# Kernel optimization log

Hardware: AMD Instinct MI355X
Metric: run time of the kernel (lower is better)

## Reference

```python
import jax, jax.numpy as jnp
import numpy as np

N_NODES = 50000
NEG_SLOPE = 0.2  # PyG GATConv default
EPS = 1e-16      # PyG softmax denominator epsilon


def _gat_conv(x, edge_index, W, att_src, att_dst, bias):
    """Single-head PyG-style GATConv with self-loops.
    x: [N, F_in], edge_index: [2, E] (row 0 = src/j, row 1 = dst/i).
    """
    n = x.shape[0]
    loop = jnp.arange(n, dtype=edge_index.dtype)
    src = jnp.concatenate([edge_index[0], loop])  # [E+N]
    dst = jnp.concatenate([edge_index[1], loop])  # [E+N]

    h = x @ W                                      # [N, F_out]
    a_src = h @ att_src                            # [N]
    a_dst = h @ att_dst                            # [N]

    e = jax.nn.leaky_relu(a_src[src] + a_dst[dst], NEG_SLOPE)  # [E+N]
    # segment softmax over incoming edges of each dst node
    m = jax.ops.segment_max(e, dst, num_segments=n)
    m = jnp.where(jnp.isfinite(m), m, 0.0)
    e = jnp.exp(e - m[dst])
    s = jax.ops.segment_sum(e, dst, num_segments=n)
    alpha = e / (s[dst] + EPS)                     # [E+N]

    out = jax.ops.segment_sum(alpha[:, None] * h[src], dst, num_segments=n)
    return out + bias


def setup_inputs() -> dict:
    key = jax.random.key(0)
    ks = jax.random.split(key, 10)
    d_in, d_hid, d_emb = 128, 64, 64
    n_edges = 800000
    x = jax.random.normal(ks[0], (N_NODES, d_in), dtype=jnp.float32)
    edge_index = jax.random.randint(ks[1], (2, n_edges), 0, N_NODES, dtype=jnp.int64)
    def glorot(k, shape):
        lim = float(np.sqrt(6.0 / sum(shape)))
        return jax.random.uniform(k, shape, jnp.float32, -lim, lim)
    return {
        "x": x,
        "edge_index": edge_index,
        "W1": glorot(ks[2], (d_in, d_hid)),
        "att_src1": glorot(ks[3], (d_hid,)),
        "att_dst1": glorot(ks[4], (d_hid,)),
        "b1": jnp.zeros((d_hid,), jnp.float32),
        "W2": glorot(ks[5], (d_hid, d_emb)),
        "att_src2": glorot(ks[6], (d_emb,)),
        "att_dst2": glorot(ks[7], (d_emb,)),
        "b2": jnp.zeros((d_emb,), jnp.float32),
    }


def reference(x, edge_index, W1, att_src1, att_dst1, b1, W2, att_src2, att_dst2, b2):
    x1 = jax.nn.relu(_gat_conv(x, edge_index, W1, att_src1, att_dst1, b1))
    # dropout is identity in eval mode
    x2 = _gat_conv(x1, edge_index, W2, att_src2, att_dst2, b2)
    return x2
```

## Files before the change

### kernel.cpp

```cpp
#include <hip/hip_runtime.h>
#include <hip/hip_bf16.h>

#define F_OUT 64
#define NEG_SLOPE 0.2f
#define SOFT_EPS 1e-16f
#define BW 256
#define CH 8192
#define TH 512

typedef short short8 __attribute__((ext_vector_type(8)));
typedef float floatx4 __attribute__((ext_vector_type(4)));
typedef unsigned short ushort4v __attribute__((ext_vector_type(4)));

__device__ __forceinline__ unsigned short f2bf_bits(float v) {
    __hip_bfloat16 hb = __float2bfloat16(v);
    return *(unsigned short*)&hb;
}
__device__ __forceinline__ float bf_bits2f(unsigned short u) {
    __hip_bfloat16 hb = *(__hip_bfloat16*)&u;
    return __bfloat162float(hb);
}
__device__ __forceinline__ float read_any(const void* src, int off, int bf) {
    return bf ? __bfloat162float(((const __hip_bfloat16*)src)[off])
              : ((const float*)src)[off];
}
__device__ __forceinline__ int get_idx(const void* ei, int i64, long long pos) {
    return i64 ? (int)((const long long*)ei)[pos] : ((const int*)ei)[pos];
}

__device__ __forceinline__ void detect_local(const unsigned* wbits, const unsigned* ebits,
                                             int* sm_bf, int* sm_i64) {
    if (threadIdx.x < 64) {
        unsigned w = wbits[threadIdx.x];
        unsigned e = (w >> 7) & 0xFFu;
        unsigned long long mb = __ballot(e >= 0x60u && e <= 0x7Eu);
        unsigned long long mz = __ballot(ebits[2 * threadIdx.x + 1] == 0u);
        if (threadIdx.x == 0) { *sm_bf = (__popcll(mb) > 32); *sm_i64 = (__popcll(mz) > 32); }
    }
    __syncthreads();
}

__global__ void count_prep(const void* __restrict__ ei, int* __restrict__ table,
                           const void* w1, const void* as1, const void* ad1, const void* b1,
                           const void* w2, const void* as2, const void* ad2, const void* b2,
                           unsigned short* __restrict__ wt1, unsigned short* __restrict__ wt2,
                           float* __restrict__ vecs, int* __restrict__ flags,
                           int E, int total, int NB, int nchunks, int n1, int n2, int K1) {
    __shared__ int cnt[1024];
    __shared__ int s_bf, s_i64;
    detect_local((const unsigned*)w1, (const unsigned*)ei, &s_bf, &s_i64);
    int bf = s_bf, i64 = s_i64;
    int g = blockIdx.x, tid = threadIdx.x;
    if (g == 0 && tid == 0) { flags[0] = bf; flags[1] = i64; }

    if (g < nchunks) {
        for (int k = tid; k < NB; k += TH) cnt[k] = 0;
        __syncthreads();
        int base = g * CH;
        int lim = base + CH < total ? base + CH : total;
        for (int t = base + tid; t < lim; t += TH) {
            int i = t < E ? get_idx(ei, i64, (long long)E + t) : t - E;
            atomicAdd(&cnt[i >> 8], 1);
        }
        __syncthreads();
        for (int k = tid; k < NB; k += TH) table[k * nchunks + g] = cnt[k];
    } else {
        int wtotal = n1 + n2 + 384;
        for (int t = tid; t < wtotal; t += TH) {
            if (t < n1) {
                int n = t / K1, k = t - n * K1;
                wt1[t] = f2bf_bits(read_any(w1, k * F_OUT + n, bf));
            } else if (t < n1 + n2) {
                int u = t - n1;
                int n = u >> 6, k = u & 63;
                wt2[u] = f2bf_bits(read_any(w2, k * F_OUT + n, bf));
            } else {
                int u = t - n1 - n2;
                const void* srcp[6] = {as1, ad1, b1, as2, ad2, b2};
                vecs[u] = read_any(srcp[u >> 6], u & 63, bf);
            }
        }
    }
}

template <int K, int WAVES>
__device__ __forceinline__ void gemm_body(int blk, int tid,
                          const void* __restrict__ xv, const unsigned short* __restrict__ Wt,
                          const float* __restrict__ att_s, const float* __restrict__ att_d,
                          unsigned short* __restrict__ h, float* __restrict__ a_s,
                          float* __restrict__ a_d, int N, int bf) {
    int lane = tid & 63;
    int m0 = (blk * WAVES + (tid >> 6)) * 16;
    if (m0 >= N) return;
    int c = lane & 15, quad = lane >> 4;
    int arow = m0 + c;
    if (arow >= N) arow = N - 1;

    floatx4 acc0 = {0.f, 0.f, 0.f, 0.f};
    floatx4 acc1 = acc0, acc2 = acc0, acc3 = acc0;

    for (int kc = 0; kc < K; kc += 32) {
        int ka = kc + quad * 8;
        short8 a;
        if (bf) {
            a = *(const short8*)((const unsigned short*)xv + (size_t)arow * K + ka);
        } else {
            const float* xp = (const float*)xv + (size_t)arow * K + ka;
#pragma unroll
            for (int j = 0; j < 8; ++j) a[j] = (short)f2bf_bits(xp[j]);
        }
        short8 b0 = *(const short8*)(Wt + (size_t)(c)      * K + ka);
        short8 b1 = *(const short8*)(Wt + (size_t)(16 + c) * K + ka);
        short8 b2 = *(const short8*)(Wt + (size_t)(32 + c) * K + ka);
        short8 b3 = *(const short8*)(Wt + (size_t)(48 + c) * K + ka);
        acc0 = __builtin_amdgcn_mfma_f32_16x16x32_bf16(a, b0, acc0, 0, 0, 0);
        acc1 = __builtin_amdgcn_mfma_f32_16x16x32_bf16(a, b1, acc1, 0, 0, 0);
        acc2 = __builtin_amdgcn_mfma_f32_16x16x32_bf16(a, b2, acc2, 0, 0, 0);
        acc3 = __builtin_amdgcn_mfma_f32_16x16x32_bf16(a, b3, acc3, 0, 0, 0);
    }

    float as0 = att_s[c],      as1 = att_s[16 + c], as2 = att_s[32 + c], as3 = att_s[48 + c];
    float ad0 = att_d[c],      ad1 = att_d[16 + c], ad2 = att_d[32 + c], ad3 = att_d[48 + c];
#pragma unroll
    for (int reg = 0; reg < 4; ++reg) {
        int row = m0 + quad * 4 + reg;
        float vs = acc0[reg] * as0 + acc1[reg] * as1 + acc2[reg] * as2 + acc3[reg] * as3;
        float vd = acc0[reg] * ad0 + acc1[reg] * ad1 + acc2[reg] * ad2 + acc3[reg] * ad3;
#pragma unroll
        for (int off = 1; off < 16; off <<= 1) {
            vs += __shfl_xor(vs, off);
            vd += __shfl_xor(vd, off);
        }
        if (row < N) {
            if (c == 0) { a_s[row] = vs; a_d[row] = vd; }
            unsigned short* hr = h + (size_t)row * F_OUT + c;
            hr[0]  = f2bf_bits(acc0[reg]);
            hr[16] = f2bf_bits(acc1[reg]);
            hr[32] = f2bf_bits(acc2[reg]);
            hr[48] = f2bf_bits(acc3[reg]);
        }
    }
}

__global__ void __launch_bounds__(TH)
scatter_gemm1(const void* __restrict__ ei, const int* __restrict__ table,
              unsigned* __restrict__ staged, int* __restrict__ segbeg,
              int* __restrict__ row_ptr, const void* __restrict__ xv,
              const unsigned short* __restrict__ Wt,
              const float* __restrict__ att_s, const float* __restrict__ att_d,
              unsigned short* __restrict__ h, float* __restrict__ a_s,
              float* __restrict__ a_d, const unsigned* __restrict__ wbits,
              int E, int total, int NB, int nchunks, int N) {
    __shared__ int s_bf, s_i64;
    detect_local(wbits, (const unsigned*)ei, &s_bf, &s_i64);
    int tid = threadIdx.x;
    if ((int)blockIdx.x >= nchunks) {
        gemm_body<128, 8>(blockIdx.x - nchunks, tid, xv, Wt, att_s, att_d,
                          h, a_s, a_d, N, s_bf);
        return;
    }
    __shared__ int s_scan[TH];
    __shared__ int s_cur[1024];
    int g = blockIdx.x;
    int i64 = s_i64;
    int b0 = 0;
    if (tid < NB) {
        const int* row = table + (size_t)tid * nchunks;
        int rsum = 0, rpart = 0;
        for (int c2 = 0; c2 < nchunks; ++c2) {
            int v = row[c2];
            rsum += v;
            rpart += (c2 < g) ? v : 0;
        }
        b0 = rsum;
        s_cur[tid] = rpart;
    }
    s_scan[tid] = (tid < NB) ? b0 : 0;
    __syncthreads();
    for (int off = 1; off < TH; off <<= 1) {
        int v = (tid >= off) ? s_scan[tid - off] : 0;
        __syncthreads();
        s_scan[tid] += v;
        __syncthreads();
    }
    if (tid < NB) {
        int excl = s_scan[tid] - b0;
        s_cur[tid] = excl + s_cur[tid];
        if (g == 0) segbeg[tid] = excl;
    }
    if (g == 0 && tid == 0) { segbeg[NB] = total; row_ptr[N] = total; }
    __syncthreads();
    int base = g * CH;
    int lim = base + CH < total ? base + CH : total;
    for (int t = base + tid; t < lim; t += TH) {
        int i = t < E ? get_idx(ei, i64, (long long)E + t) : t - E;
        int j = t < E ? get_idx(ei, i64, t) : t - E;
        int pos = atomicAdd(&s_cur[i >> 8], 1);
        staged[pos] = ((unsigned)(i & 255) << 24) | (unsigned)j;
    }
}

__global__ void bucket_csr(const unsigned* __restrict__ staged, const int* __restrict__ segbeg,
                           int* __restrict__ row_ptr, int* __restrict__ eidx, int N) {
    __shared__ int ldeg[BW];
    __shared__ int lcur[BW];
    __shared__ int wtot[4];
    int b = blockIdx.x;
    int t = threadIdx.x;
    int seg_beg = segbeg[b];
    int seg_end = segbeg[b + 1];
    ldeg[t] = 0;
    __syncthreads();
    for (int p = seg_beg + t; p < seg_end; p += 256)
        atomicAdd(&ldeg[staged[p] >> 24], 1);
    __syncthreads();
    int lane = t & 63, w = t >> 6;
    int d = ldeg[t];
    int v = d;
#pragma unroll
    for (int off = 1; off < 64; off <<= 1) {
        int u = __shfl_up(v, off);
        if (lane >= off) v += u;
    }
    if (lane == 63) wtot[w] = v;
    __syncthreads();
    int woff = 0;
    for (int k = 0; k < w; ++k) woff += wtot[k];
    int excl = v - d + woff;
    int node = b * BW + t;
    if (node < N) row_ptr[node] = seg_beg + excl;
    lcur[t] = excl;
    __syncthreads();
    for (int p = seg_beg + t; p < seg_end; p += 256) {
        unsigned pk = staged[p];
        int pos = atomicAdd(&lcur[pk >> 24], 1);
        eidx[seg_beg + pos] = (int)(pk & 0xFFFFFFu);
    }
}

__device__ __forceinline__ void gather_node(int i, int lane, int quad, int c,
                                            const int* __restrict__ row_ptr,
                                            const int* __restrict__ eidx,
                                            const float* __restrict__ a_s,
                                            const float* __restrict__ a_d,
                                            const unsigned short* __restrict__ h,
                                            float* se_out, floatx4* A_out) {
    int beg = row_ptr[i];
    int end = row_ptr[i + 1];
    float ad = a_d[i];
    float se = 0.f;
    floatx4 acc[4];
#pragma unroll
    for (int k = 0; k < 4; ++k) acc[k] = (floatx4){0.f, 0.f, 0.f, 0.f};

    for (int p = beg; p < end; p += 64) {
        int tile = end - p; if (tile > 64) tile = 64;
        int jm = eidx[p + (lane < tile ? lane : tile - 1)];
        float wm = 0.f;
        if (lane < tile) {
            float e = a_s[jm] + ad;
            wm = __expf(e > 0.f ? e : NEG_SLOPE * e);
        }
        se += wm;
        for (int e = 0; e < tile; e += 16) {
#pragma unroll
            for (int k = 0; k < 4; ++k) {
                if (e + 4 * k < tile) {
                    int idx = e + 4 * k + quad;
                    int srcl = idx < tile ? idx : tile - 1;
                    int jk = __shfl(jm, srcl);
                    float wk = __shfl(wm, srcl);
                    if (idx >= tile) wk = 0.f;
                    ushort4v hv = *(const ushort4v*)(h + (size_t)jk * F_OUT + (c << 2));
                    acc[k][0] += wk * bf_bits2f(hv[0]);
                    acc[k][1] += wk * bf_bits2f(hv[1]);
                    acc[k][2] += wk * bf_bits2f(hv[2]);
                    acc[k][3] += wk * bf_bits2f(hv[3]);
                }
            }
        }
    }
#pragma unroll
    for (int off = 1; off < 64; off <<= 1) se += __shfl_xor(se, off);
    floatx4 A = (acc[0] + acc[1]) + (acc[2] + acc[3]);
#pragma unroll
    for (int m = 0; m < 4; ++m) {
        A[m] += __shfl_xor(A[m], 16);
        A[m] += __shfl_xor(A[m], 32);
    }
    *se_out = se;
    *A_out = A;
}

#define XST 72
__global__ void __launch_bounds__(1024)
gather1_gemm2(const int* __restrict__ row_ptr, const int* __restrict__ eidx,
              const float* __restrict__ a_s, const float* __restrict__ a_d,
              const unsigned short* __restrict__ h, const float* __restrict__ bias,
              const unsigned short* __restrict__ Wt2,
              const float* __restrict__ att_s2, const float* __restrict__ att_d2,
              unsigned short* __restrict__ h2, float* __restrict__ a_s2,
              float* __restrict__ a_d2, int N) {
    __shared__ unsigned short x1t[16 * XST];
    int tid = threadIdx.x;
    int lane = tid & 63;
    int wv = tid >> 6;
    int quad = lane >> 4, c = lane & 15;
    int i = blockIdx.x * 16 + wv;

    if (i < N) {
        float se; floatx4 A;
        gather_node(i, lane, quad, c, row_ptr, eidx, a_s, a_d, h, &se, &A);
        if (quad == 0) {
            int col = c << 2;
            float inv = 1.f / (se + SOFT_EPS);
            float v0 = A[0] * inv + bias[col];
            float v1 = A[1] * inv + bias[col + 1];
            float v2 = A[2] * inv + bias[col + 2];
            float v3 = A[3] * inv + bias[col + 3];
            ushort4v ov;
            ov[0] = f2bf_bits(v0 > 0.f ? v0 : 0.f);
            ov[1] = f2bf_bits(v1 > 0.f ? v1 : 0.f);
            ov[2] = f2bf_bits(v2 > 0.f ? v2 : 0.f);
            ov[3] = f2bf_bits(v3 > 0.f ? v3 : 0.f);
            *(ushort4v*)(x1t + wv * XST + col) = ov;
        }
    } else if (quad == 0) {
        *(ushort4v*)(x1t + wv * XST + (c << 2)) = (ushort4v){0, 0, 0, 0};
    }
    __syncthreads();

    if (wv == 0) {
        int m0 = blockIdx.x * 16;
        floatx4 acc0 = {0.f, 0.f, 0.f, 0.f};
        floatx4 acc1 = acc0, acc2 = acc0, acc3 = acc0;
#pragma unroll
        for (int kc = 0; kc < 64; kc += 32) {
            int ka = kc + quad * 8;
            short8 a = *(const short8*)(x1t + c * XST + ka);
            short8 b0 = *(const short8*)(Wt2 + (size_t)(c)      * 64 + ka);
            short8 b1 = *(const short8*)(Wt2 + (size_t)(16 + c) * 64 + ka);
            short8 b2 = *(const short8*)(Wt2 + (size_t)(32 + c) * 64 + ka);
            short8 b3 = *(const short8*)(Wt2 + (size_t)(48 + c) * 64 + ka);
            acc0 = __builtin_amdgcn_mfma_f32_16x16x32_bf16(a, b0, acc0, 0, 0, 0);
            acc1 = __builtin_amdgcn_mfma_f32_16x16x32_bf16(a, b1, acc1, 0, 0, 0);
            acc2 = __builtin_amdgcn_mfma_f32_16x16x32_bf16(a, b2, acc2, 0, 0, 0);
            acc3 = __builtin_amdgcn_mfma_f32_16x16x32_bf16(a, b3, acc3, 0, 0, 0);
        }
        float as0 = att_s2[c],      as1 = att_s2[16 + c], as2 = att_s2[32 + c], as3 = att_s2[48 + c];
        float ad0 = att_d2[c],      ad1 = att_d2[16 + c], ad2 = att_d2[32 + c], ad3 = att_d2[48 + c];
#pragma unroll
        for (int reg = 0; reg < 4; ++reg) {
            int row = m0 + quad * 4 + reg;
            float vs = acc0[reg] * as0 + acc1[reg] * as1 + acc2[reg] * as2 + acc3[reg] * as3;
            float vd = acc0[reg] * ad0 + acc1[reg] * ad1 + acc2[reg] * ad2 + acc3[reg] * ad3;
#pragma unroll
            for (int off = 1; off < 16; off <<= 1) {
                vs += __shfl_xor(vs, off);
                vd += __shfl_xor(vd, off);
            }
            if (row < N) {
                if (c == 0) { a_s2[row] = vs; a_d2[row] = vd; }
                unsigned short* hr = h2 + (size_t)row * F_OUT + c;
                hr[0]  = f2bf_bits(acc0[reg]);
                hr[16] = f2bf_bits(acc1[reg]);
                hr[32] = f2bf_bits(acc2[reg]);
                hr[48] = f2bf_bits(acc3[reg]);
            }
        }
    }
}

__global__ void node_gather_out(const int* __restrict__ row_ptr, const int* __restrict__ eidx,
                                const float* __restrict__ a_s, const float* __restrict__ a_d,
                                const unsigned short* __restrict__ h, const float* __restrict__ bias,
                                void* __restrict__ out, int N, const int* __restrict__ flags) {
    int lane = threadIdx.x & 63;
    int i = blockIdx.x * 4 + (threadIdx.x >> 6);
    if (i >= N) return;
    int quad = lane >> 4, c = lane & 15;
    float se; floatx4 A;
    gather_node(i, lane, quad, c, row_ptr, eidx, a_s, a_d, h, &se, &A);
    if (quad == 0) {
        int col = c << 2;
        float inv = 1.f / (se + SOFT_EPS);
        float v0 = A[0] * inv + bias[col];
        float v1 = A[1] * inv + bias[col + 1];
        float v2 = A[2] * inv + bias[col + 2];
        float v3 = A[3] * inv + bias[col + 3];
        size_t o = (size_t)i * F_OUT + col;
        if (flags[0]) {
            ushort4v ov;
            ov[0] = f2bf_bits(v0); ov[1] = f2bf_bits(v1);
            ov[2] = f2bf_bits(v2); ov[3] = f2bf_bits(v3);
            *(ushort4v*)((unsigned short*)out + o) = ov;
        } else {
            floatx4 ov = {v0, v1, v2, v3};
            *(floatx4*)((float*)out + o) = ov;
        }
    }
}

extern "C" void kernel_launch(void* const* d_in, const int* in_sizes, int n_in,
                              void* d_out, int out_size, void* d_ws, size_t ws_size,
                              hipStream_t stream) {
    const void* x   = d_in[0];
    const void* ei  = d_in[1];
    const void* W1  = d_in[2];
    const void* as1 = d_in[3];
    const void* ad1 = d_in[4];
    const void* b1  = d_in[5];
    const void* W2  = d_in[6];
    const void* as2 = d_in[7];
    const void* ad2 = d_in[8];
    const void* b2  = d_in[9];

    int E  = in_sizes[1] / 2;
    int n1 = in_sizes[2];
    int n2 = in_sizes[6];
    int K1 = n1 / F_OUT;
    int N  = in_sizes[0] / K1;
    int total = E + N;
    int NB = (N + BW - 1) / BW;
    int nchunks = (total + CH - 1) / CH;
    int M = NB * nchunks;

    size_t nf = (size_t)N * F_OUT;
    char* wsb = (char*)d_ws;
    unsigned short* h   = (unsigned short*)wsb;
    unsigned short* h2  = h + nf;
    unsigned short* wt1 = h2 + nf;
    unsigned short* wt2 = wt1 + n1;
    float* a_s  = (float*)(wt2 + n2 + ((n1 + n2) & 1));
    float* a_d  = a_s + N;
    float* a_s2 = a_d + N;
    float* a_d2 = a_s2 + N;
    float* vecs = a_d2 + N;
    float* cAs1 = vecs,       *cAd1 = vecs + 64,  *cB1 = vecs + 128;
    float* cAs2 = vecs + 192, *cAd2 = vecs + 256, *cB2 = vecs + 320;
    int* flags    = (int*)(vecs + 384);
    int* row_ptr  = flags + 8;
    int* eidx     = row_ptr + N + 1;
    unsigned* staged = (unsigned*)(eidx + total);
    int* table    = (int*)(staged + total);
    int* segbeg   = table + M;

    int blkG1 = (N + 127) / 128;
    int blkFuse = (N + 15) / 16;
    int blkNode = (N + 3) / 4;

    count_prep<<<nchunks + 1, TH, 0, stream>>>(ei, table, W1, as1, ad1, b1,
                                               W2, as2, ad2, b2, wt1, wt2, vecs, flags,
                                               E, total, NB, nchunks, n1, n2, K1);
    scatter_gemm1<<<nchunks + blkG1, TH, 0, stream>>>(ei, table, staged, segbeg, row_ptr,
                                                      x, wt1, cAs1, cAd1, h, a_s, a_d,
                                                      (const unsigned*)W1,
                                                      E, total, NB, nchunks, N);
    bucket_csr<<<NB, 256, 0, stream>>>(staged, segbeg, row_ptr, eidx, N);
    gather1_gemm2<<<blkFuse, 1024, 0, stream>>>(row_ptr, eidx, a_s, a_d, h, cB1,
                                                wt2, cAs2, cAd2, h2, a_s2, a_d2, N);
    node_gather_out<<<blkNode, 256, 0, stream>>>(row_ptr, eidx, a_s2, a_d2, h2, cB2,
                                                 d_out, N, flags);
}
```

Baseline: 203.6 us.

## Split per-node edge gather into 8 edge groups with 16-byte feature loads

The per-node gather now gives each wave's 8 lane groups a contiguous slice of the node's incoming edges. Each lane loads 8 bf16 features at once and every lane computes its own attention weights, replacing the earlier tile-and-shuffle scheme that used 4-wide loads. Partial sums are combined with xor shuffles at the end. The CSR bucketing kernel also moves to 512 threads per block to speed up the scatter loops. The intent is fewer shuffles and wider memory transactions, at the cost of more redundant exp work per edge and possible imbalance on low-degree nodes.

```diff
diff --git a/kernel.cpp b/kernel.cpp
--- a/kernel.cpp
+++ b/kernel.cpp
@@ -7,10 +7,12 @@
 #define BW 256
 #define CH 8192
 #define TH 512
+#define TH3 512
 
 typedef short short8 __attribute__((ext_vector_type(8)));
 typedef float floatx4 __attribute__((ext_vector_type(4)));
 typedef unsigned short ushort4v __attribute__((ext_vector_type(4)));
+typedef unsigned short ushort8v __attribute__((ext_vector_type(8)));
 
 __device__ __forceinline__ unsigned short f2bf_bits(float v) {
     __hip_bfloat16 hb = __float2bfloat16(v);
@@ -200,8 +202,9 @@
     }
 }
 
-__global__ void bucket_csr(const unsigned* __restrict__ staged, const int* __restrict__ segbeg,
-                           int* __restrict__ row_ptr, int* __restrict__ eidx, int N) {
+__global__ void __launch_bounds__(TH3)
+bucket_csr(const unsigned* __restrict__ staged, const int* __restrict__ segbeg,
+           int* __restrict__ row_ptr, int* __restrict__ eidx, int N) {
     __shared__ int ldeg[BW];
     __shared__ int lcur[BW];
     __shared__ int wtot[4];
@@ -209,87 +212,89 @@
     int t = threadIdx.x;
     int seg_beg = segbeg[b];
     int seg_end = segbeg[b + 1];
-    ldeg[t] = 0;
-    __syncthreads();
-    for (int p = seg_beg + t; p < seg_end; p += 256)
+    if (t < BW) ldeg[t] = 0;
+    __syncthreads();
+    for (int p = seg_beg + t; p < seg_end; p += TH3)
         atomicAdd(&ldeg[staged[p] >> 24], 1);
     __syncthreads();
     int lane = t & 63, w = t >> 6;
-    int d = ldeg[t];
-    int v = d;
-#pragma unroll
-    for (int off = 1; off < 64; off <<= 1) {
-        int u = __shfl_up(v, off);
-        if (lane >= off) v += u;
-    }
-    if (lane == 63) wtot[w] = v;
-    __syncthreads();
-    int woff = 0;
-    for (int k = 0; k < w; ++k) woff += wtot[k];
-    int excl = v - d + woff;
-    int node = b * BW + t;
-    if (node < N) row_ptr[node] = seg_beg + excl;
-    lcur[t] = excl;
-    __syncthreads();
-    for (int p = seg_beg + t; p < seg_end; p += 256) {
+    int d = 0, v = 0;
+    if (t < BW) {
+        d = ldeg[t];
+        v = d;
+#pragma unroll
+        for (int off = 1; off < 64; off <<= 1) {
+            int u = __shfl_up(v, off);
+            if (lane >= off) v += u;
+        }
+        if (lane == 63) wtot[w] = v;
+    }
+    __syncthreads();
+    if (t < BW) {
+        int woff = 0;
+        for (int k = 0; k < w; ++k) woff += wtot[k];
+        int excl = v - d + woff;
+        int node = b * BW + t;
+        if (node < N) row_ptr[node] = seg_beg + excl;
+        lcur[t] = excl;
+    }
+    __syncthreads();
+    for (int p = seg_beg + t; p < seg_end; p += TH3) {
         unsigned pk = staged[p];
         int pos = atomicAdd(&lcur[pk >> 24], 1);
         eidx[seg_beg + pos] = (int)(pk & 0xFFFFFFu);
     }
 }
 
-__device__ __forceinline__ void gather_node(int i, int lane, int quad, int c,
-                                            const int* __restrict__ row_ptr,
-                                            const int* __restrict__ eidx,
-                                            const float* __restrict__ a_s,
-                                            const float* __restrict__ a_d,
-                                            const unsigned short* __restrict__ h,
-                                            float* se_out, floatx4* A_out) {
+__device__ __forceinline__ void gather_node8(int i, int grp, int c8,
+                                             const int* __restrict__ row_ptr,
+                                             const int* __restrict__ eidx,
+                                             const float* __restrict__ a_s,
+                                             const float* __restrict__ a_d,
+                                             const unsigned short* __restrict__ h,
+                                             float* se_out, float acc[8]) {
     int beg = row_ptr[i];
     int end = row_ptr[i + 1];
+    int len = end - beg;
     float ad = a_d[i];
+    int gb = beg + ((len * grp) >> 3);
+    int ge = beg + ((len * (grp + 1)) >> 3);
     float se = 0.f;
-    floatx4 acc[4];
-#pragma unroll
-    for (int k = 0; k < 4; ++k) acc[k] = (floatx4){0.f, 0.f, 0.f, 0.f};
-
-    for (int p = beg; p < end; p += 64) {
-        int tile = end - p; if (tile > 64) tile = 64;
-        int jm = eidx[p + (lane < tile ? lane : tile - 1)];
-        float wm = 0.f;
-        if (lane < tile) {
-            float e = a_s[jm] + ad;
-            wm = __expf(e > 0.f ? e : NEG_SLOPE * e);
-        }
-        se += wm;
-        for (int e = 0; e < tile; e += 16) {
-#pragma unroll
-            for (int k = 0; k < 4; ++k) {
-                if (e + 4 * k < tile) {
-                    int idx = e + 4 * k + quad;
-                    int srcl = idx < tile ? idx : tile - 1;
-                    int jk = __shfl(jm, srcl);
-                    float wk = __shfl(wm, srcl);
-                    if (idx >= tile) wk = 0.f;
-                    ushort4v hv = *(const ushort4v*)(h + (size_t)jk * F_OUT + (c << 2));
-                    acc[k][0] += wk * bf_bits2f(hv[0]);
-                    acc[k][1] += wk * bf_bits2f(hv[1]);
-                    acc[k][2] += wk * bf_bits2f(hv[2]);
-                    acc[k][3] += wk * bf_bits2f(hv[3]);
-                }
-            }
-        }
-    }
-#pragma unroll
-    for (int off = 1; off < 64; off <<= 1) se += __shfl_xor(se, off);
-    floatx4 A = (acc[0] + acc[1]) + (acc[2] + acc[3]);
-#pragma unroll
-    for (int m = 0; m < 4; ++m) {
-        A[m] += __shfl_xor(A[m], 16);
-        A[m] += __shfl_xor(A[m], 32);
+#pragma unroll
+    for (int k = 0; k < 8; ++k) acc[k] = 0.f;
+
+    int p = gb;
+    for (; p + 1 < ge; p += 2) {
+        int j0 = eidx[p];
+        int j1 = eidx[p + 1];
+        ushort8v hv0 = *(const ushort8v*)(h + (((size_t)j0) << 6) + (c8 << 3));
+        ushort8v hv1 = *(const ushort8v*)(h + (((size_t)j1) << 6) + (c8 << 3));
+        float e0 = a_s[j0] + ad;
+        float e1 = a_s[j1] + ad;
+        float w0 = __expf(fmaxf(e0, NEG_SLOPE * e0));
+        float w1 = __expf(fmaxf(e1, NEG_SLOPE * e1));
+        se += w0 + w1;
+#pragma unroll
+        for (int k = 0; k < 8; ++k)
+            acc[k] += w0 * bf_bits2f(hv0[k]) + w1 * bf_bits2f(hv1[k]);
+    }
+    if (p < ge) {
+        int j0 = eidx[p];
+        ushort8v hv0 = *(const ushort8v*)(h + (((size_t)j0) << 6) + (c8 << 3));
+        float e0 = a_s[j0] + ad;
+        float w0 = __expf(fmaxf(e0, NEG_SLOPE * e0));
+        se += w0;
+#pragma unroll
+        for (int k = 0; k < 8; ++k) acc[k] += w0 * bf_bits2f(hv0[k]);
+    }
+
+#pragma unroll
+    for (int off = 8; off < 64; off <<= 1) {
+        se += __shfl_xor(se, off);
+#pragma unroll
+        for (int k = 0; k < 8; ++k) acc[k] += __shfl_xor(acc[k], off);
     }
     *se_out = se;
-    *A_out = A;
 }
 
 #define XST 72
@@ -305,32 +310,30 @@
     int tid = threadIdx.x;
     int lane = tid & 63;
     int wv = tid >> 6;
-    int quad = lane >> 4, c = lane & 15;
+    int grp = lane >> 3, c8 = lane & 7;
     int i = blockIdx.x * 16 + wv;
 
     if (i < N) {
-        float se; floatx4 A;
-        gather_node(i, lane, quad, c, row_ptr, eidx, a_s, a_d, h, &se, &A);
-        if (quad == 0) {
-            int col = c << 2;
+        float se, acc[8];
+        gather_node8(i, grp, c8, row_ptr, eidx, a_s, a_d, h, &se, acc);
+        if (grp == 0) {
+            int col = c8 << 3;
             float inv = 1.f / (se + SOFT_EPS);
-            float v0 = A[0] * inv + bias[col];
-            float v1 = A[1] * inv + bias[col + 1];
-            float v2 = A[2] * inv + bias[col + 2];
-            float v3 = A[3] * inv + bias[col + 3];
-            ushort4v ov;
-            ov[0] = f2bf_bits(v0 > 0.f ? v0 : 0.f);
-            ov[1] = f2bf_bits(v1 > 0.f ? v1 : 0.f);
-            ov[2] = f2bf_bits(v2 > 0.f ? v2 : 0.f);
-            ov[3] = f2bf_bits(v3 > 0.f ? v3 : 0.f);
-            *(ushort4v*)(x1t + wv * XST + col) = ov;
-        }
-    } else if (quad == 0) {
-        *(ushort4v*)(x1t + wv * XST + (c << 2)) = (ushort4v){0, 0, 0, 0};
+            ushort8v ov;
+#pragma unroll
+            for (int k = 0; k < 8; ++k) {
+                float v = acc[k] * inv + bias[col + k];
+                ov[k] = f2bf_bits(v > 0.f ? v : 0.f);
+            }
+            *(ushort8v*)(x1t + wv * XST + col) = ov;
+        }
+    } else if (grp == 0) {
+        *(ushort8v*)(x1t + wv * XST + (c8 << 3)) = (ushort8v){0, 0, 0, 0, 0, 0, 0, 0};
     }
     __syncthreads();
 
     if (wv == 0) {
+        int quad = lane >> 4, c = lane & 15;
         int m0 = blockIdx.x * 16;
         floatx4 acc0 = {0.f, 0.f, 0.f, 0.f};
         floatx4 acc1 = acc0, acc2 = acc0, acc3 = acc0;
@@ -371,32 +374,34 @@
     }
 }
 
-__global__ void node_gather_out(const int* __restrict__ row_ptr, const int* __restrict__ eidx,
-                                const float* __restrict__ a_s, const float* __restrict__ a_d,
-                                const unsigned short* __restrict__ h, const float* __restrict__ bias,
-                                void* __restrict__ out, int N, const int* __restrict__ flags) {
+__global__ void __launch_bounds__(256)
+node_gather_out(const int* __restrict__ row_ptr, const int* __restrict__ eidx,
+                const float* __restrict__ a_s, const float* __restrict__ a_d,
+                const unsigned short* __restrict__ h, const float* __restrict__ bias,
+                void* __restrict__ out, int N, const int* __restrict__ flags) {
     int lane = threadIdx.x & 63;
     int i = blockIdx.x * 4 + (threadIdx.x >> 6);
     if (i >= N) return;
-    int quad = lane >> 4, c = lane & 15;
-    float se; floatx4 A;
-    gather_node(i, lane, quad, c, row_ptr, eidx, a_s, a_d, h, &se, &A);
-    if (quad == 0) {
-        int col = c << 2;
+    int grp = lane >> 3, c8 = lane & 7;
+    float se, acc[8];
+    gather_node8(i, grp, c8, row_ptr, eidx, a_s, a_d, h, &se, acc);
+    if (grp == 0) {
+        int col = c8 << 3;
         float inv = 1.f / (se + SOFT_EPS);
-        float v0 = A[0] * inv + bias[col];
-        float v1 = A[1] * inv + bias[col + 1];
-        float v2 = A[2] * inv + bias[col + 2];
-        float v3 = A[3] * inv + bias[col + 3];
+        float v[8];
+#pragma unroll
+        for (int k = 0; k < 8; ++k) v[k] = acc[k] * inv + bias[col + k];
         size_t o = (size_t)i * F_OUT + col;
         if (flags[0]) {
-            ushort4v ov;
-            ov[0] = f2bf_bits(v0); ov[1] = f2bf_bits(v1);
-            ov[2] = f2bf_bits(v2); ov[3] = f2bf_bits(v3);
-            *(ushort4v*)((unsigned short*)out + o) = ov;
+            ushort8v ov;
+#pragma unroll
+            for (int k = 0; k < 8; ++k) ov[k] = f2bf_bits(v[k]);
+            *(ushort8v*)((unsigned short*)out + o) = ov;
         } else {
-            floatx4 ov = {v0, v1, v2, v3};
-            *(floatx4*)((float*)out + o) = ov;
+            floatx4 o0 = {v[0], v[1], v[2], v[3]};
+            floatx4 o1 = {v[4], v[5], v[6], v[7]};
+            *(floatx4*)((float*)out + o) = o0;
+            *(floatx4*)((float*)out + o + 4) = o1;
         }
     }
 }
@@ -456,7 +461,7 @@
                                                       x, wt1, cAs1, cAd1, h, a_s, a_d,
                                                       (const unsigned*)W1,
                                                       E, total, NB, nchunks, N);
-    bucket_csr<<<NB, 256, 0, stream>>>(staged, segbeg, row_ptr, eidx, N);
+    bucket_csr<<<NB, TH3, 0, stream>>>(staged, segbeg, row_ptr, eidx, N);
     gather1_gemm2<<<blkFuse, 1024, 0, stream>>>(row_ptr, eidx, a_s, a_d, h, cB1,
                                                 wt2, cAs2, cAd2, h2, a_s2, a_d2, N);
     node_gather_out<<<blkNode, 256, 0, stream>>>(row_ptr, eidx, a_s2, a_d2, h2, cB2,
```

New measurement: 188.7 us. 7.4% less time.
